# Kernel optimization log

Measured on AMD Instinct MI355X. Metric: run time of the kernel, lower is better.

The kernel has to match this reference:

```python
import jax, jax.numpy as jnp
from jax import lax
import numpy as np

C = 16          # channels
K = 3           # deformable kernel size
PAD = 1


def conv3(x, w, b):
    # 3x3 SAME conv, NCHW / OIHW
    y = lax.conv_general_dilated(x, w, (1, 1), 'SAME',
                                 dimension_numbers=('NCHW', 'OIHW', 'NCHW'))
    return y + b[None, :, None, None]


def deform_conv2d(x, offsets, mask, w, b):
    """torchvision-style modulated deformable conv, stride=1, pad=1, dil=1.
    x: [B,C,H,W]; offsets: [B,2*K*K,H,W] (per-tap y,x interleaved);
    mask: [B,K*K,H,W]; w: [Cout,C,K,K]; b: [Cout]."""
    B, Cin, H, W = x.shape
    ky, kx = jnp.meshgrid(jnp.arange(K), jnp.arange(K), indexing='ij')
    ky = ky.reshape(-1).astype(x.dtype)   # [9]
    kx = kx.reshape(-1).astype(x.dtype)
    off = offsets.reshape(B, K * K, 2, H, W)  # off[:,k,0]=dy, off[:,k,1]=dx
    hh = jnp.arange(H, dtype=x.dtype)
    ww = jnp.arange(W, dtype=x.dtype)
    py = hh[None, None, :, None] + (ky - PAD)[None, :, None, None] + off[:, :, 0]  # [B,9,H,W]
    px = ww[None, None, None, :] + (kx - PAD)[None, :, None, None] + off[:, :, 1]
    y0 = jnp.floor(py)
    x0 = jnp.floor(px)
    dy = py - y0
    dx = px - x0

    def sample_one(img, y0b, x0b, dyb, dxb):
        # img [C,H,W]; y0b/x0b/dyb/dxb [9,H,W]
        y0i = y0b.astype(jnp.int32)
        x0i = x0b.astype(jnp.int32)

        def gather(yi, xi):
            valid = ((yi >= 0) & (yi < H) & (xi >= 0) & (xi < W)).astype(img.dtype)
            yc = jnp.clip(yi, 0, H - 1)
            xc = jnp.clip(xi, 0, W - 1)
            return img[:, yc, xc] * valid[None]   # [C,9,H,W]

        v00 = gather(y0i,     x0i)
        v01 = gather(y0i,     x0i + 1)
        v10 = gather(y0i + 1, x0i)
        v11 = gather(y0i + 1, x0i + 1)
        return (v00 * (1 - dyb) * (1 - dxb) + v01 * (1 - dyb) * dxb
                + v10 * dyb * (1 - dxb) + v11 * dyb * dxb)   # [C,9,H,W]

    sampled = jax.vmap(sample_one)(x, y0, x0, dy, dx)          # [B,C,9,H,W]
    sampled = sampled * mask[:, None]                           # modulate
    out = jnp.einsum('bckhw,ock->bohw', sampled, w.reshape(w.shape[0], Cin, K * K))
    return out + b[None, :, None, None]


def setup_inputs() -> dict:
    key = jax.random.key(0)
    ks = iter(jax.random.split(key, 32))

    def w(shape, scale=0.1):
        return (jax.random.normal(next(ks), shape, dtype=jnp.float32) * scale)

    B, H, W = 4, 256, 256
    d = {
        'f_E': jax.random.normal(next(ks), (B, C, H, W), dtype=jnp.float32),
        'f_F': jax.random.normal(next(ks), (B, C, H, W), dtype=jnp.float32),
        # SpatialAttentionBlock
        'sab_att_w1': w((C, 2 * C, 3, 3)), 'sab_att_b1': w((C,)),
        'sab_att_w2': w((1, C, 3, 3)),      'sab_att_b2': w((1,)),
        'sab_ref_w':  w((C, 2 * C, 3, 3)),  'sab_ref_b':  w((C,)),
        # DeformableConvLayer offset/mask net (last layer small -> modest offsets)
        'om_w1': w((C, 2 * C, 3, 3)),       'om_b1': w((C,)),
        'om_w2': w((C, C, 3, 3)),           'om_b2': w((C,)),
        'om_w3': w((3 * K * K, C, 3, 3), 0.05), 'om_b3': w((3 * K * K,), 0.05),
        # deformable conv weight/bias
        'dcb_w': w((C, C, 3, 3)),           'dcb_b': w((C,)),
        # refinements
        'dcbref_w': w((C, 2 * C, 3, 3)),    'dcbref_b': w((C,)),
        'fin_w':    w((C, 2 * C, 3, 3)),    'fin_b':    w((C,)),
    }
    return d


def reference(f_E, f_F,
              sab_att_w1, sab_att_b1, sab_att_w2, sab_att_b2,
              sab_ref_w, sab_ref_b,
              om_w1, om_b1, om_w2, om_b2, om_w3, om_b3,
              dcb_w, dcb_b, dcbref_w, dcbref_b, fin_w, fin_b):
    relu = jax.nn.relu
    # --- SAB branch: sab(f_E, f_F) ---
    comb = jnp.concatenate([f_E, f_F], axis=1)
    M_E = jax.nn.sigmoid(conv3(relu(conv3(comb, sab_att_w1, sab_att_b1)),
                               sab_att_w2, sab_att_b2))          # [B,1,H,W]
    f_Esa = f_E * M_E
    f_EFsa = relu(conv3(jnp.concatenate([f_Esa, f_F], axis=1), sab_ref_w, sab_ref_b))
    # --- DCB branch: dcb_layer(f_F, f_E) -> deform on f_E, cat([f_E, f_F]) ---
    comb2 = jnp.concatenate([f_E, f_F], axis=1)
    om = conv3(relu(conv3(relu(conv3(comb2, om_w1, om_b1)), om_w2, om_b2)),
               om_w3, om_b3)                                      # [B,27,H,W]
    offsets = om[:, :2 * K * K]
    mask = jax.nn.sigmoid(om[:, 2 * K * K:])
    f_Edc = relu(deform_conv2d(f_E, offsets, mask, dcb_w, dcb_b))
    f_EFdc = relu(conv3(jnp.concatenate([f_Edc, f_F], axis=1), dcbref_w, dcbref_b))
    # --- final fusion ---
    f_EF = relu(conv3(jnp.concatenate([f_EFsa, f_EFdc], axis=1), fin_w, fin_b))
    return f_EF
```

## Files before the change

kernel.cpp:

```cpp
#include <hip/hip_runtime.h>
#include <cstdint>
#include <cstddef>

#define HH 256
#define WW 256
#define HWW (HH * WW)

typedef __attribute__((ext_vector_type(8))) short bf16x8;
typedef __attribute__((ext_vector_type(4))) float f32x4;

__device__ inline unsigned short f2bf(float f) {
  unsigned u = __float_as_uint(f);
  unsigned r = (u + 0x7fffu + ((u >> 16) & 1u)) >> 16;
  return (unsigned short)r;
}
__device__ inline float bf2f(unsigned short u) {
  return __uint_as_float((unsigned)u << 16);
}
__device__ inline float bf_lo(unsigned w) { return __uint_as_float(w << 16); }
__device__ inline float bf_hi(unsigned w) { return __uint_as_float(w & 0xffff0000u); }

struct RD { const float* src; void* dst; int cin, cout, mode; };
struct RA { RD d[9]; };

__device__ void repack_one(const RD& t) {
  if (t.mode == 2) {
    const int NST = (t.cin * 9 + 31) / 32;
    const int OT = (t.cout + 15) / 16;
    const int n = OT * NST * 512;
    unsigned short* dst = (unsigned short*)t.dst;
    for (int i = threadIdx.x; i < n; i += 256) {
      int j = i & 7;
      int l = (i >> 3) & 63;
      int rest = i >> 9;
      int s = rest % NST;
      int ot = rest / NST;
      int o = ot * 16 + (l & 15);
      int klin = s * 32 + ((l >> 4) << 3) + j;
      int tap = klin / t.cin;
      int c = klin % t.cin;
      float v = 0.f;
      if (tap < 9 && o < t.cout) v = t.src[(o * t.cin + c) * 9 + tap];
      dst[i] = f2bf(v);
    }
  } else {
    float* dst = (float*)t.dst;
    const int n = t.cin * t.cout * 9;
    for (int i = threadIdx.x; i < n; i += 256) {
      int k = i % 9;
      int rest = i / 9;
      int c = rest % t.cin;
      int o = rest / t.cin;
      if (t.mode == 0) dst[(c * 9 + k) * t.cout + o] = t.src[(o * t.cin + c) * 9 + k];
      else             dst[(k * t.cin + c) * t.cout + o] = t.src[(o * t.cin + c) * 9 + k];
    }
  }
}

__global__ __launch_bounds__(256) void prep_k(
    RA ra, const float* __restrict__ fe, const float* __restrict__ ff,
    unsigned short* __restrict__ xe, unsigned short* __restrict__ xf) {
  const int b = blockIdx.z;
  if (blockIdx.x == 256) {
    const int d0 = b * 3;
    for (int d = d0; d < d0 + 3 && d < 9; ++d) repack_one(ra.d[d]);
    return;
  }
  const int pixel = blockIdx.x * 256 + threadIdx.x;
#pragma unroll
  for (int t = 0; t < 2; ++t) {
    const float* src = t ? ff : fe;
    unsigned short* dst = t ? xf : xe;
    unsigned w[8];
#pragma unroll
    for (int j = 0; j < 8; ++j) {
      unsigned short lo = f2bf(src[((size_t)b * 16 + 2 * j) * HWW + pixel]);
      unsigned short hi = f2bf(src[((size_t)b * 16 + 2 * j + 1) * HWW + pixel]);
      w[j] = (unsigned)lo | ((unsigned)hi << 16);
    }
    uint4* d4 = (uint4*)(dst + ((size_t)b * HWW + pixel) * 16);
    d4[0] = make_uint4(w[0], w[1], w[2], w[3]);
    d4[1] = make_uint4(w[4], w[5], w[6], w[7]);
  }
}

template <int NSLOT, int OT, int OUT_MODE, int COUTR>
__global__ __launch_bounds__(256) void conv_nhwc(
    const unsigned short* __restrict__ inA, const unsigned short* __restrict__ inB,
    const unsigned short* __restrict__ wtm, const float* __restrict__ bias,
    void* __restrict__ outv) {
  constexpr int CIN = NSLOT * 8;
  constexpr int NST = (CIN * 9 + 31) / 32;
  constexpr int SHIFT = (NSLOT == 4) ? 1 : 2;
  constexpr int STRIDE = NSLOT * 16;
  constexpr int PX = 34, PY = 10;
  __shared__ __align__(16) char smem[PY * PX * STRIDE];

  const int b = blockIdx.z;
  const int tx0 = blockIdx.x * 32;
  const int ty0 = blockIdx.y * 8;
  const int tid = threadIdx.x;
  const int lane = tid & 63;
  const int wv = tid >> 6;

  bf16x8 afr[OT][NST];
#pragma unroll
  for (int ot = 0; ot < OT; ++ot)
#pragma unroll
    for (int s = 0; s < NST; ++s)
      afr[ot][s] = *(const bf16x8*)(wtm + (size_t)(((ot * NST + s) * 64 + lane) * 8));

  const int px_l = lane & 15;
  const int og = lane >> 4;

  f32x4 acc[4][OT];
#pragma unroll
  for (int ot = 0; ot < OT; ++ot) {
    f32x4 bv;
#pragma unroll
    for (int r = 0; r < 4; ++r) {
      int o = ot * 16 + og * 4 + r;
      bv[r] = bias[o < COUTR ? o : COUTR - 1];
    }
#pragma unroll
    for (int t = 0; t < 4; ++t) acc[t][ot] = bv;
  }

  for (int i = tid; i < PY * PX * NSLOT; i += 256) {
    int pp = i / NSLOT;
    int s = i - pp * NSLOT;
    int ly = pp / PX;
    int lx = pp - ly * PX;
    int gy = ty0 + ly - 1;
    int gx = tx0 + lx - 1;
    uint4 v = make_uint4(0, 0, 0, 0);
    if (gy >= 0 && gy < HH && gx >= 0 && gx < WW) {
      const unsigned short* src = (NSLOT == 2 || s < 2) ? inA : inB;
      int sl = (NSLOT == 4 && s >= 2) ? s - 2 : s;
      v = *(const uint4*)(src + ((size_t)b * HWW + (size_t)gy * WW + gx) * 16 + sl * 8);
    }
    int swz = (s ^ (pp >> SHIFT)) & (NSLOT - 1);
    *(uint4*)(smem + (size_t)pp * STRIDE + (swz << 4)) = v;
  }
  __syncthreads();

  int dpix[NST], dslot[NST];
#pragma unroll
  for (int s = 0; s < NST; ++s) {
    int klin = s * 32 + og * 8;
    int tap = klin / CIN;
    if (tap > 8) tap = 8;
    int coff = klin % CIN;
    dpix[s] = (tap / 3) * PX + (tap % 3);
    dslot[s] = coff >> 3;
  }

  const int oy_l = wv * 2;
#pragma unroll
  for (int t = 0; t < 4; ++t) {
    const int base_pix = (oy_l + (t >> 1)) * PX + (t & 1) * 16 + px_l;
#pragma unroll
    for (int s = 0; s < NST; ++s) {
      int pp = base_pix + dpix[s];
      int off = pp * STRIDE + (((dslot[s] ^ (pp >> SHIFT)) & (NSLOT - 1)) << 4);
      bf16x8 bvv = *(const bf16x8*)(smem + off);
#pragma unroll
      for (int ot = 0; ot < OT; ++ot)
        acc[t][ot] = __builtin_amdgcn_mfma_f32_16x16x32_bf16(afr[ot][s], bvv, acc[t][ot], 0, 0, 0);
    }
  }

#pragma unroll
  for (int t = 0; t < 4; ++t) {
    const int gy = ty0 + oy_l + (t >> 1);
    const int gx = tx0 + (t & 1) * 16 + px_l;
#pragma unroll
    for (int ot = 0; ot < OT; ++ot) {
      const int o0 = ot * 16 + og * 4;
      if (OUT_MODE == 2) {
        unsigned lo = (unsigned)f2bf(fmaxf(acc[t][ot][0], 0.f)) |
                      ((unsigned)f2bf(fmaxf(acc[t][ot][1], 0.f)) << 16);
        unsigned hi = (unsigned)f2bf(fmaxf(acc[t][ot][2], 0.f)) |
                      ((unsigned)f2bf(fmaxf(acc[t][ot][3], 0.f)) << 16);
        uint2* dst = (uint2*)((unsigned short*)outv +
                              ((size_t)b * HWW + (size_t)gy * WW + gx) * 16 + o0);
        *dst = make_uint2(lo, hi);
      } else if (OUT_MODE == 0) {
#pragma unroll
        for (int r = 0; r < 4; ++r) {
          int o = o0 + r;
          if (o < COUTR)
            ((float*)outv)[((size_t)b * COUTR + o) * HWW + (size_t)gy * WW + gx] =
                fmaxf(acc[t][ot][r], 0.f);
        }
      } else {
#pragma unroll
        for (int r = 0; r < 4; ++r) {
          int o = o0 + r;
          if (o < COUTR)
            ((unsigned short*)outv)[((size_t)b * COUTR + o) * HWW + (size_t)gy * WW + gx] =
                f2bf(acc[t][ot][r]);
        }
      }
    }
  }
}

__global__ __launch_bounds__(256) void conv_dual_k(
    const unsigned short* __restrict__ inA, const unsigned short* __restrict__ inB,
    const unsigned short* __restrict__ w1, const float* __restrict__ b1,
    const unsigned short* __restrict__ w2, const float* __restrict__ b2,
    unsigned short* __restrict__ out1, unsigned short* __restrict__ out2) {
  constexpr int NSLOT = 4, NST = 9, SHIFT = 1, STRIDE = 64, PX = 34, PY = 10;
  __shared__ __align__(16) char smem[PY * PX * STRIDE];

  const int b = blockIdx.z;
  const int tx0 = blockIdx.x * 32;
  const int ty0 = blockIdx.y * 8;
  const int tid = threadIdx.x;
  const int lane = tid & 63;
  const int wv = tid >> 6;

  bf16x8 afr1[NST], afr2[NST];
#pragma unroll
  for (int s = 0; s < NST; ++s) {
    afr1[s] = *(const bf16x8*)(w1 + (size_t)((s * 64 + lane) * 8));
    afr2[s] = *(const bf16x8*)(w2 + (size_t)((s * 64 + lane) * 8));
  }

  const int px_l = lane & 15;
  const int og = lane >> 4;

  f32x4 acc1[4], acc2[4];
  {
    f32x4 bv1, bv2;
#pragma unroll
    for (int r = 0; r < 4; ++r) {
      bv1[r] = b1[og * 4 + r];
      bv2[r] = b2[og * 4 + r];
    }
#pragma unroll
    for (int t = 0; t < 4; ++t) { acc1[t] = bv1; acc2[t] = bv2; }
  }

  for (int i = tid; i < PY * PX * NSLOT; i += 256) {
    int pp = i / NSLOT;
    int s = i - pp * NSLOT;
    int ly = pp / PX;
    int lx = pp - ly * PX;
    int gy = ty0 + ly - 1;
    int gx = tx0 + lx - 1;
    uint4 v = make_uint4(0, 0, 0, 0);
    if (gy >= 0 && gy < HH && gx >= 0 && gx < WW) {
      const unsigned short* src = (s < 2) ? inA : inB;
      int sl = (s >= 2) ? s - 2 : s;
      v = *(const uint4*)(src + ((size_t)b * HWW + (size_t)gy * WW + gx) * 16 + sl * 8);
    }
    int swz = (s ^ (pp >> SHIFT)) & 3;
    *(uint4*)(smem + (size_t)pp * STRIDE + (swz << 4)) = v;
  }
  __syncthreads();

  int dpix[NST], dslot[NST];
#pragma unroll
  for (int s = 0; s < NST; ++s) {
    int klin = s * 32 + og * 8;
    int tap = klin / 32;
    int coff = klin % 32;
    dpix[s] = (tap / 3) * PX + (tap % 3);
    dslot[s] = coff >> 3;
  }

  const int oy_l = wv * 2;
#pragma unroll
  for (int t = 0; t < 4; ++t) {
    const int base_pix = (oy_l + (t >> 1)) * PX + (t & 1) * 16 + px_l;
#pragma unroll
    for (int s = 0; s < NST; ++s) {
      int pp = base_pix + dpix[s];
      int off = pp * STRIDE + (((dslot[s] ^ (pp >> SHIFT)) & 3) << 4);
      bf16x8 bvv = *(const bf16x8*)(smem + off);
      acc1[t] = __builtin_amdgcn_mfma_f32_16x16x32_bf16(afr1[s], bvv, acc1[t], 0, 0, 0);
      acc2[t] = __builtin_amdgcn_mfma_f32_16x16x32_bf16(afr2[s], bvv, acc2[t], 0, 0, 0);
    }
  }

#pragma unroll
  for (int t = 0; t < 4; ++t) {
    const int gy = ty0 + oy_l + (t >> 1);
    const int gx = tx0 + (t & 1) * 16 + px_l;
    const size_t base = ((size_t)b * HWW + (size_t)gy * WW + gx) * 16 + og * 4;
    {
      unsigned lo = (unsigned)f2bf(fmaxf(acc1[t][0], 0.f)) |
                    ((unsigned)f2bf(fmaxf(acc1[t][1], 0.f)) << 16);
      unsigned hi = (unsigned)f2bf(fmaxf(acc1[t][2], 0.f)) |
                    ((unsigned)f2bf(fmaxf(acc1[t][3], 0.f)) << 16);
      *(uint2*)(out1 + base) = make_uint2(lo, hi);
    }
    {
      unsigned lo = (unsigned)f2bf(fmaxf(acc2[t][0], 0.f)) |
                    ((unsigned)f2bf(fmaxf(acc2[t][1], 0.f)) << 16);
      unsigned hi = (unsigned)f2bf(fmaxf(acc2[t][2], 0.f)) |
                    ((unsigned)f2bf(fmaxf(acc2[t][3], 0.f)) << 16);
      *(uint2*)(out2 + base) = make_uint2(lo, hi);
    }
  }
}

__global__ __launch_bounds__(256) void sagate_k(
    const unsigned short* __restrict__ xa, const unsigned short* __restrict__ xe,
    const unsigned short* __restrict__ xf,
    const float* __restrict__ gw, const float* __restrict__ gb,
    const unsigned short* __restrict__ wtm, const float* __restrict__ bias,
    unsigned short* __restrict__ out) {
  constexpr int NST = 9, SHIFT = 1, STRIDE = 64, PX = 34, PY = 10;
  __shared__ __align__(16) char smem[PY * PX * STRIDE];

  const int b = blockIdx.z;
  const int tx0 = blockIdx.x * 32;
  const int ty0 = blockIdx.y * 8;
  const int tid = threadIdx.x;
  const int lane = tid & 63;
  const int wv = tid >> 6;

  bf16x8 afr[NST];
#pragma unroll
  for (int s = 0; s < NST; ++s)
    afr[s] = *(const bf16x8*)(wtm + (size_t)((s * 64 + lane) * 8));

  const int px_l = lane & 15;
  const int og = lane >> 4;

  f32x4 acc[4];
  {
    f32x4 bv;
#pragma unroll
    for (int r = 0; r < 4; ++r) bv[r] = bias[og * 4 + r];
#pragma unroll
    for (int t = 0; t < 4; ++t) acc[t] = bv;
  }

  for (int i = tid; i < PY * PX * 2; i += 256) {
    int pp = i >> 1;
    int s = 2 + (i & 1);
    int ly = pp / PX;
    int lx = pp - ly * PX;
    int gy = ty0 + ly - 1;
    int gx = tx0 + lx - 1;
    uint4 v = make_uint4(0, 0, 0, 0);
    if (gy >= 0 && gy < HH && gx >= 0 && gx < WW)
      v = *(const uint4*)(xf + ((size_t)b * HWW + (size_t)gy * WW + gx) * 16 + (s - 2) * 8);
    int swz = (s ^ (pp >> SHIFT)) & 3;
    *(uint4*)(smem + (size_t)pp * STRIDE + (swz << 4)) = v;
  }

  const float gbias = gb[0];
  for (int i = tid; i < PY * PX; i += 256) {
    int ly = i / PX;
    int lx = i - ly * PX;
    int gy = ty0 + ly - 1;
    int gx = tx0 + lx - 1;
    uint4 v0 = make_uint4(0, 0, 0, 0), v1 = make_uint4(0, 0, 0, 0);
    if (gy >= 0 && gy < HH && gx >= 0 && gx < WW) {
      float a = gbias;
#pragma unroll
      for (int ky = 0; ky < 3; ++ky) {
        int ay = gy + ky - 1;
        if (ay < 0 || ay >= HH) continue;
#pragma unroll
        for (int kx = 0; kx < 3; ++kx) {
          int ax = gx + kx - 1;
          if (ax < 0 || ax >= WW) continue;
          const int k = ky * 3 + kx;
          const uint4* p = (const uint4*)(xa + ((size_t)b * HWW + (size_t)ay * WW + ax) * 16);
          uint4 t0 = p[0], t1 = p[1];
          unsigned wv8[8] = {t0.x, t0.y, t0.z, t0.w, t1.x, t1.y, t1.z, t1.w};
#pragma unroll
          for (int j = 0; j < 8; ++j) {
            a = fmaf(bf_lo(wv8[j]), gw[(2 * j) * 9 + k], a);
            a = fmaf(bf_hi(wv8[j]), gw[(2 * j + 1) * 9 + k], a);
          }
        }
      }
      float m = 1.0f / (1.0f + expf(-a));
      const uint4* pe = (const uint4*)(xe + ((size_t)b * HWW + (size_t)gy * WW + gx) * 16);
      uint4 e0 = pe[0], e1 = pe[1];
      unsigned ev[8] = {e0.x, e0.y, e0.z, e0.w, e1.x, e1.y, e1.z, e1.w};
      unsigned r[8];
#pragma unroll
      for (int j = 0; j < 8; ++j) {
        unsigned short lo = f2bf(bf_lo(ev[j]) * m);
        unsigned short hi = f2bf(bf_hi(ev[j]) * m);
        r[j] = (unsigned)lo | ((unsigned)hi << 16);
      }
      v0 = make_uint4(r[0], r[1], r[2], r[3]);
      v1 = make_uint4(r[4], r[5], r[6], r[7]);
    }
    int swz0 = (0 ^ (i >> SHIFT)) & 3;
    int swz1 = (1 ^ (i >> SHIFT)) & 3;
    *(uint4*)(smem + (size_t)i * STRIDE + (swz0 << 4)) = v0;
    *(uint4*)(smem + (size_t)i * STRIDE + (swz1 << 4)) = v1;
  }
  __syncthreads();

  int dpix[NST], dslot[NST];
#pragma unroll
  for (int s = 0; s < NST; ++s) {
    int klin = s * 32 + og * 8;
    int tap = klin / 32;
    int coff = klin % 32;
    dpix[s] = (tap / 3) * PX + (tap % 3);
    dslot[s] = coff >> 3;
  }

  const int oy_l = wv * 2;
#pragma unroll
  for (int t = 0; t < 4; ++t) {
    const int base_pix = (oy_l + (t >> 1)) * PX + (t & 1) * 16 + px_l;
#pragma unroll
    for (int s = 0; s < NST; ++s) {
      int pp = base_pix + dpix[s];
      int off = pp * STRIDE + (((dslot[s] ^ (pp >> SHIFT)) & 3) << 4);
      bf16x8 bvv = *(const bf16x8*)(smem + off);
      acc[t] = __builtin_amdgcn_mfma_f32_16x16x32_bf16(afr[s], bvv, acc[t], 0, 0, 0);
    }
  }

#pragma unroll
  for (int t = 0; t < 4; ++t) {
    const int gy = ty0 + oy_l + (t >> 1);
    const int gx = tx0 + (t & 1) * 16 + px_l;
    unsigned lo = (unsigned)f2bf(fmaxf(acc[t][0], 0.f)) |
                  ((unsigned)f2bf(fmaxf(acc[t][1], 0.f)) << 16);
    unsigned hi = (unsigned)f2bf(fmaxf(acc[t][2], 0.f)) |
                  ((unsigned)f2bf(fmaxf(acc[t][3], 0.f)) << 16);
    *(uint2*)(out + ((size_t)b * HWW + (size_t)gy * WW + gx) * 16 + og * 4) = make_uint2(lo, hi);
  }
}

__global__ __launch_bounds__(256) void deform_v4(
    const unsigned short* __restrict__ xn, const unsigned short* __restrict__ om,
    const float* __restrict__ wt, const float* __restrict__ bias,
    unsigned short* __restrict__ out) {
  const int bid = blockIdx.x;
  const int xcd = bid & 7;
  const int b = xcd >> 1;
  const int pb = ((bid >> 3) << 1) | (xcd & 1);
  const int pixel = pb * 256 + (int)threadIdx.x;
  const int y = pixel >> 8;
  const int xq = pixel & 255;
  const unsigned short* xb = xn + (size_t)b * HWW * 16;
  const unsigned short* omb = om + (size_t)b * 27 * HWW;

  float acc[16];
#pragma unroll
  for (int o = 0; o < 16; ++o) acc[o] = bias[o];

#pragma unroll
  for (int k = 0; k < 9; ++k) {
    float offy = bf2f(omb[(size_t)(2 * k) * HWW + pixel]);
    float offx = bf2f(omb[(size_t)(2 * k + 1) * HWW + pixel]);
    float m = 1.0f / (1.0f + expf(-bf2f(omb[(size_t)(18 + k) * HWW + pixel])));
    float py = (float)y + (float)(k / 3 - 1) + offy;
    float px = (float)xq + (float)(k % 3 - 1) + offx;
    float y0f = floorf(py);
    float x0f = floorf(px);
    float dy = py - y0f;
    float dx = px - x0f;
    int y0 = (int)y0f, x0 = (int)x0f;
    int y1 = y0 + 1, x1 = x0 + 1;
    bool vy0 = (y0 >= 0) && (y0 < HH);
    bool vy1 = (y1 >= 0) && (y1 < HH);
    bool vx0 = (x0 >= 0) && (x0 < WW);
    bool vx1 = (x1 >= 0) && (x1 < WW);
    int yc0 = min(max(y0, 0), HH - 1);
    int yc1 = min(max(y1, 0), HH - 1);
    int xc0 = min(max(x0, 0), WW - 1);
    int xc1 = min(max(x1, 0), WW - 1);
    float w00 = (1.f - dy) * (1.f - dx) * m;
    float w01 = (1.f - dy) * dx * m;
    float w10 = dy * (1.f - dx) * m;
    float w11 = dy * dx * m;
    if (!(vy0 && vx0)) w00 = 0.f;
    if (!(vy0 && vx1)) w01 = 0.f;
    if (!(vy1 && vx0)) w10 = 0.f;
    if (!(vy1 && vx1)) w11 = 0.f;

    const uint4* p00 = (const uint4*)(xb + (size_t)(yc0 * WW + xc0) * 16);
    const uint4* p01 = (const uint4*)(xb + (size_t)(yc0 * WW + xc1) * 16);
    const uint4* p10 = (const uint4*)(xb + (size_t)(yc1 * WW + xc0) * 16);
    const uint4* p11 = (const uint4*)(xb + (size_t)(yc1 * WW + xc1) * 16);
    uint4 a0 = p00[0], a1 = p00[1];
    uint4 b0 = p01[0], b1 = p01[1];
    uint4 c0 = p10[0], c1 = p10[1];
    uint4 d0 = p11[0], d1 = p11[1];
    unsigned wA[8] = {a0.x, a0.y, a0.z, a0.w, a1.x, a1.y, a1.z, a1.w};
    unsigned wB[8] = {b0.x, b0.y, b0.z, b0.w, b1.x, b1.y, b1.z, b1.w};
    unsigned wC[8] = {c0.x, c0.y, c0.z, c0.w, c1.x, c1.y, c1.z, c1.w};
    unsigned wD[8] = {d0.x, d0.y, d0.z, d0.w, d1.x, d1.y, d1.z, d1.w};

    float s[16];
#pragma unroll
    for (int j = 0; j < 8; ++j) {
      s[2 * j]     = bf_lo(wA[j]) * w00 + bf_lo(wB[j]) * w01 + bf_lo(wC[j]) * w10 + bf_lo(wD[j]) * w11;
      s[2 * j + 1] = bf_hi(wA[j]) * w00 + bf_hi(wB[j]) * w01 + bf_hi(wC[j]) * w10 + bf_hi(wD[j]) * w11;
    }
    const float* wk = wt + (size_t)k * 256;
#pragma unroll
    for (int c = 0; c < 16; ++c)
#pragma unroll
      for (int o = 0; o < 16; ++o)
        acc[o] = fmaf(s[c], wk[c * 16 + o], acc[o]);
  }
  unsigned r[8];
#pragma unroll
  for (int j = 0; j < 8; ++j) {
    unsigned short lo = f2bf(fmaxf(acc[2 * j], 0.f));
    unsigned short hi = f2bf(fmaxf(acc[2 * j + 1], 0.f));
    r[j] = (unsigned)lo | ((unsigned)hi << 16);
  }
  uint4* d4 = (uint4*)(out + ((size_t)b * HWW + pixel) * 16);
  d4[0] = make_uint4(r[0], r[1], r[2], r[3]);
  d4[1] = make_uint4(r[4], r[5], r[6], r[7]);
}

extern "C" void kernel_launch(void* const* d_in, const int* in_sizes, int n_in,
                              void* d_out, int out_size, void* d_ws, size_t ws_size,
                              hipStream_t stream) {
  (void)in_sizes; (void)n_in; (void)out_size; (void)ws_size;
  const float* f_E = (const float*)d_in[0];
  const float* f_F = (const float*)d_in[1];
  const float* att_w1 = (const float*)d_in[2];
  const float* att_b1 = (const float*)d_in[3];
  const float* att_w2 = (const float*)d_in[4];
  const float* att_b2 = (const float*)d_in[5];
  const float* ref_w = (const float*)d_in[6];
  const float* ref_b = (const float*)d_in[7];
  const float* om_w1 = (const float*)d_in[8];
  const float* om_b1 = (const float*)d_in[9];
  const float* om_w2 = (const float*)d_in[10];
  const float* om_b2 = (const float*)d_in[11];
  const float* om_w3 = (const float*)d_in[12];
  const float* om_b3 = (const float*)d_in[13];
  const float* dcb_w = (const float*)d_in[14];
  const float* dcb_b = (const float*)d_in[15];
  const float* dcbref_w = (const float*)d_in[16];
  const float* dcbref_b = (const float*)d_in[17];
  const float* fin_w = (const float*)d_in[18];
  const float* fin_b = (const float*)d_in[19];
  float* outp = (float*)d_out;

  const size_t TN = (size_t)4 * HWW * 16;
  unsigned short* XE  = (unsigned short*)d_ws;
  unsigned short* XF  = XE + TN;
  unsigned short* XA  = XF + TN;
  unsigned short* XT  = XA + TN;
  unsigned short* X2  = XT + TN;
  unsigned short* XSA = X2 + TN;
  unsigned short* OMB = XSA + TN;
  unsigned short* WM  = OMB + (size_t)4 * 27 * HWW;

  unsigned short* WM_att1 = WM;
  unsigned short* WM_ref  = WM_att1 + 4608;
  unsigned short* WM_om1  = WM_ref + 4608;
  unsigned short* WM_om2  = WM_om1 + 4608;
  unsigned short* WM_om3  = WM_om2 + 2560;
  unsigned short* WM_dref = WM_om3 + 5120;
  unsigned short* WM_fin  = WM_dref + 4608;
  float* WF_att2 = (float*)(WM_fin + 4608);
  float* WF_dcb  = WF_att2 + 144;

  RA ra;
  ra.d[0] = {att_w1, WM_att1, 32, 16, 2};
  ra.d[1] = {ref_w, WM_ref, 32, 16, 2};
  ra.d[2] = {om_w1, WM_om1, 32, 16, 2};
  ra.d[3] = {om_w2, WM_om2, 16, 16, 2};
  ra.d[4] = {om_w3, WM_om3, 16, 27, 2};
  ra.d[5] = {dcbref_w, WM_dref, 32, 16, 2};
  ra.d[6] = {fin_w, WM_fin, 32, 16, 2};
  ra.d[7] = {att_w2, WF_att2, 16, 1, 0};
  ra.d[8] = {dcb_w, WF_dcb, 16, 16, 1};

  dim3 blk(256);
  prep_k<<<dim3(257, 1, 4), blk, 0, stream>>>(ra, f_E, f_F, XE, XF);

  dim3 gm(WW / 32, HH / 8, 4);

  conv_dual_k<<<gm, blk, 0, stream>>>(XE, XF, WM_att1, att_b1, WM_om1, om_b1, XA, XT);
  sagate_k<<<gm, blk, 0, stream>>>(XA, XE, XF, WF_att2, att_b2, WM_ref, ref_b, X2);
  conv_nhwc<2, 1, 2, 16><<<gm, blk, 0, stream>>>(XT, nullptr, WM_om2, om_b2, XA);
  conv_nhwc<2, 2, 1, 27><<<gm, blk, 0, stream>>>(XA, nullptr, WM_om3, om_b3, OMB);
  deform_v4<<<dim3(1024), blk, 0, stream>>>(XE, OMB, WF_dcb, dcb_b, XSA);
  conv_nhwc<4, 1, 2, 16><<<gm, blk, 0, stream>>>(XSA, XF, WM_dref, dcbref_b, XT);
  conv_nhwc<4, 1, 0, 16><<<gm, blk, 0, stream>>>(X2, XT, WM_fin, fin_b, outp);
}
```

Baseline: 115.4 us.

## Fuse consecutive 3x3 conv pairs into halo-recomputing kernels

Replaces the separate om2→om3 convolutions and the dcbref→final convolutions with two fused kernels. Each computes the first conv over a tile enlarged by a one-pixel halo and keeps the intermediate in LDS, then runs the second conv from LDS. This drops two kernel launches and the global write and read of two intermediate bf16 tensors. In exchange it recomputes halo pixels, uses more shared memory per block (which may lower occupancy), and adds an extra barrier phase.

```diff
diff --git a/kernel.cpp b/kernel.cpp
--- a/kernel.cpp
+++ b/kernel.cpp
@@ -84,128 +84,6 @@
   }
 }
 
-template <int NSLOT, int OT, int OUT_MODE, int COUTR>
-__global__ __launch_bounds__(256) void conv_nhwc(
-    const unsigned short* __restrict__ inA, const unsigned short* __restrict__ inB,
-    const unsigned short* __restrict__ wtm, const float* __restrict__ bias,
-    void* __restrict__ outv) {
-  constexpr int CIN = NSLOT * 8;
-  constexpr int NST = (CIN * 9 + 31) / 32;
-  constexpr int SHIFT = (NSLOT == 4) ? 1 : 2;
-  constexpr int STRIDE = NSLOT * 16;
-  constexpr int PX = 34, PY = 10;
-  __shared__ __align__(16) char smem[PY * PX * STRIDE];
-
-  const int b = blockIdx.z;
-  const int tx0 = blockIdx.x * 32;
-  const int ty0 = blockIdx.y * 8;
-  const int tid = threadIdx.x;
-  const int lane = tid & 63;
-  const int wv = tid >> 6;
-
-  bf16x8 afr[OT][NST];
-#pragma unroll
-  for (int ot = 0; ot < OT; ++ot)
-#pragma unroll
-    for (int s = 0; s < NST; ++s)
-      afr[ot][s] = *(const bf16x8*)(wtm + (size_t)(((ot * NST + s) * 64 + lane) * 8));
-
-  const int px_l = lane & 15;
-  const int og = lane >> 4;
-
-  f32x4 acc[4][OT];
-#pragma unroll
-  for (int ot = 0; ot < OT; ++ot) {
-    f32x4 bv;
-#pragma unroll
-    for (int r = 0; r < 4; ++r) {
-      int o = ot * 16 + og * 4 + r;
-      bv[r] = bias[o < COUTR ? o : COUTR - 1];
-    }
-#pragma unroll
-    for (int t = 0; t < 4; ++t) acc[t][ot] = bv;
-  }
-
-  for (int i = tid; i < PY * PX * NSLOT; i += 256) {
-    int pp = i / NSLOT;
-    int s = i - pp * NSLOT;
-    int ly = pp / PX;
-    int lx = pp - ly * PX;
-    int gy = ty0 + ly - 1;
-    int gx = tx0 + lx - 1;
-    uint4 v = make_uint4(0, 0, 0, 0);
-    if (gy >= 0 && gy < HH && gx >= 0 && gx < WW) {
-      const unsigned short* src = (NSLOT == 2 || s < 2) ? inA : inB;
-      int sl = (NSLOT == 4 && s >= 2) ? s - 2 : s;
-      v = *(const uint4*)(src + ((size_t)b * HWW + (size_t)gy * WW + gx) * 16 + sl * 8);
-    }
-    int swz = (s ^ (pp >> SHIFT)) & (NSLOT - 1);
-    *(uint4*)(smem + (size_t)pp * STRIDE + (swz << 4)) = v;
-  }
-  __syncthreads();
-
-  int dpix[NST], dslot[NST];
-#pragma unroll
-  for (int s = 0; s < NST; ++s) {
-    int klin = s * 32 + og * 8;
-    int tap = klin / CIN;
-    if (tap > 8) tap = 8;
-    int coff = klin % CIN;
-    dpix[s] = (tap / 3) * PX + (tap % 3);
-    dslot[s] = coff >> 3;
-  }
-
-  const int oy_l = wv * 2;
-#pragma unroll
-  for (int t = 0; t < 4; ++t) {
-    const int base_pix = (oy_l + (t >> 1)) * PX + (t & 1) * 16 + px_l;
-#pragma unroll
-    for (int s = 0; s < NST; ++s) {
-      int pp = base_pix + dpix[s];
-      int off = pp * STRIDE + (((dslot[s] ^ (pp >> SHIFT)) & (NSLOT - 1)) << 4);
-      bf16x8 bvv = *(const bf16x8*)(smem + off);
-#pragma unroll
-      for (int ot = 0; ot < OT; ++ot)
-        acc[t][ot] = __builtin_amdgcn_mfma_f32_16x16x32_bf16(afr[ot][s], bvv, acc[t][ot], 0, 0, 0);
-    }
-  }
-
-#pragma unroll
-  for (int t = 0; t < 4; ++t) {
-    const int gy = ty0 + oy_l + (t >> 1);
-    const int gx = tx0 + (t & 1) * 16 + px_l;
-#pragma unroll
-    for (int ot = 0; ot < OT; ++ot) {
-      const int o0 = ot * 16 + og * 4;
-      if (OUT_MODE == 2) {
-        unsigned lo = (unsigned)f2bf(fmaxf(acc[t][ot][0], 0.f)) |
-                      ((unsigned)f2bf(fmaxf(acc[t][ot][1], 0.f)) << 16);
-        unsigned hi = (unsigned)f2bf(fmaxf(acc[t][ot][2], 0.f)) |
-                      ((unsigned)f2bf(fmaxf(acc[t][ot][3], 0.f)) << 16);
-        uint2* dst = (uint2*)((unsigned short*)outv +
-                              ((size_t)b * HWW + (size_t)gy * WW + gx) * 16 + o0);
-        *dst = make_uint2(lo, hi);
-      } else if (OUT_MODE == 0) {
-#pragma unroll
-        for (int r = 0; r < 4; ++r) {
-          int o = o0 + r;
-          if (o < COUTR)
-            ((float*)outv)[((size_t)b * COUTR + o) * HWW + (size_t)gy * WW + gx] =
-                fmaxf(acc[t][ot][r], 0.f);
-        }
-      } else {
-#pragma unroll
-        for (int r = 0; r < 4; ++r) {
-          int o = o0 + r;
-          if (o < COUTR)
-            ((unsigned short*)outv)[((size_t)b * COUTR + o) * HWW + (size_t)gy * WW + gx] =
-                f2bf(acc[t][ot][r]);
-        }
-      }
-    }
-  }
-}
-
 __global__ __launch_bounds__(256) void conv_dual_k(
     const unsigned short* __restrict__ inA, const unsigned short* __restrict__ inB,
     const unsigned short* __restrict__ w1, const float* __restrict__ b1,
@@ -435,6 +313,147 @@
     unsigned hi = (unsigned)f2bf(fmaxf(acc[t][2], 0.f)) |
                   ((unsigned)f2bf(fmaxf(acc[t][3], 0.f)) << 16);
     *(uint2*)(out + ((size_t)b * HWW + (size_t)gy * WW + gx) * 16 + og * 4) = make_uint2(lo, hi);
+  }
+}
+
+__global__ __launch_bounds__(256) void om_fused_k(
+    const unsigned short* __restrict__ xt,
+    const unsigned short* __restrict__ w2m, const float* __restrict__ b2,
+    const unsigned short* __restrict__ w3m, const float* __restrict__ b3,
+    unsigned short* __restrict__ omb) {
+  __shared__ __align__(16) char smem[12 * 36 * 32 + 10 * 34 * 32];
+  char* stage = smem;
+  char* t3 = smem + 12 * 36 * 32;
+
+  const int b = blockIdx.z;
+  const int tx0 = blockIdx.x * 32;
+  const int ty0 = blockIdx.y * 8;
+  const int tid = threadIdx.x;
+  const int lane = tid & 63;
+  const int wv = tid >> 6;
+  const int px_l = lane & 15;
+  const int og = lane >> 4;
+
+  for (int i = tid; i < 12 * 36 * 2; i += 256) {
+    int pp = i >> 1;
+    int s = i & 1;
+    int lr = pp / 36;
+    int lc = pp - lr * 36;
+    int gy = ty0 + lr - 2;
+    int gx = tx0 + lc - 2;
+    uint4 v = make_uint4(0, 0, 0, 0);
+    if (gy >= 0 && gy < HH && gx >= 0 && gx < WW)
+      v = *(const uint4*)(xt + ((size_t)b * HWW + (size_t)gy * WW + gx) * 16 + s * 8);
+    int swz = (s ^ (pp >> 2)) & 1;
+    *(uint4*)(stage + (size_t)pp * 32 + (swz << 4)) = v;
+  }
+  __syncthreads();
+
+  {
+    bf16x8 afr1[5];
+#pragma unroll
+    for (int s = 0; s < 5; ++s)
+      afr1[s] = *(const bf16x8*)(w2m + (size_t)((s * 64 + lane) * 8));
+    f32x4 bvec;
+#pragma unroll
+    for (int r = 0; r < 4; ++r) bvec[r] = b2[og * 4 + r];
+    int tap1[5], slot1[5];
+#pragma unroll
+    for (int s = 0; s < 5; ++s) {
+      int klin = s * 32 + og * 8;
+      int tap = klin / 16;
+      if (tap > 8) tap = 8;
+      int coff = klin % 16;
+      tap1[s] = (tap / 3) * 36 + (tap % 3);
+      slot1[s] = coff >> 3;
+    }
+    for (int f = wv; f < 22; f += 4) {
+      int p = f * 16 + px_l;
+      int r = p / 34;
+      int c = p - r * 34;
+      f32x4 acc = bvec;
+#pragma unroll
+      for (int s = 0; s < 5; ++s) {
+        int pp2 = r * 36 + c + tap1[s];
+        int off = pp2 * 32 + (((slot1[s] ^ (pp2 >> 2)) & 1) << 4);
+        bf16x8 bv = *(const bf16x8*)(stage + off);
+        acc = __builtin_amdgcn_mfma_f32_16x16x32_bf16(afr1[s], bv, acc, 0, 0, 0);
+      }
+      if (p < 340) {
+        int gy = ty0 + r - 1;
+        int gx = tx0 + c - 1;
+        unsigned lo = 0, hi = 0;
+        if (gy >= 0 && gy < HH && gx >= 0 && gx < WW) {
+          lo = (unsigned)f2bf(fmaxf(acc[0], 0.f)) | ((unsigned)f2bf(fmaxf(acc[1], 0.f)) << 16);
+          hi = (unsigned)f2bf(fmaxf(acc[2], 0.f)) | ((unsigned)f2bf(fmaxf(acc[3], 0.f)) << 16);
+        }
+        int slot = og >> 1;
+        int off = p * 32 + (((slot ^ (p >> 2)) & 1) << 4) + (og & 1) * 8;
+        *(uint2*)(t3 + off) = make_uint2(lo, hi);
+      }
+    }
+  }
+  __syncthreads();
+
+  bf16x8 afr2[2][5];
+#pragma unroll
+  for (int ot = 0; ot < 2; ++ot)
+#pragma unroll
+    for (int s = 0; s < 5; ++s)
+      afr2[ot][s] = *(const bf16x8*)(w3m + (size_t)(((ot * 5 + s) * 64 + lane) * 8));
+
+  f32x4 acc2[4][2];
+#pragma unroll
+  for (int ot = 0; ot < 2; ++ot) {
+    f32x4 bv;
+#pragma unroll
+    for (int r = 0; r < 4; ++r) {
+      int o = ot * 16 + og * 4 + r;
+      bv[r] = b3[o < 27 ? o : 26];
+    }
+#pragma unroll
+    for (int t = 0; t < 4; ++t) acc2[t][ot] = bv;
+  }
+
+  int tap2[5], slot2[5];
+#pragma unroll
+  for (int s = 0; s < 5; ++s) {
+    int klin = s * 32 + og * 8;
+    int tap = klin / 16;
+    if (tap > 8) tap = 8;
+    int coff = klin % 16;
+    tap2[s] = (tap / 3) * 34 + (tap % 3);
+    slot2[s] = coff >> 3;
+  }
+
+  const int oy_l = wv * 2;
+#pragma unroll
+  for (int t = 0; t < 4; ++t) {
+    const int base_pix = (oy_l + (t >> 1)) * 34 + (t & 1) * 16 + px_l;
+#pragma unroll
+    for (int s = 0; s < 5; ++s) {
+      int pp = base_pix + tap2[s];
+      int off = pp * 32 + (((slot2[s] ^ (pp >> 2)) & 1) << 4);
+      bf16x8 bv = *(const bf16x8*)(t3 + off);
+      acc2[t][0] = __builtin_amdgcn_mfma_f32_16x16x32_bf16(afr2[0][s], bv, acc2[t][0], 0, 0, 0);
+      acc2[t][1] = __builtin_amdgcn_mfma_f32_16x16x32_bf16(afr2[1][s], bv, acc2[t][1], 0, 0, 0);
+    }
+  }
+
+#pragma unroll
+  for (int t = 0; t < 4; ++t) {
+    const int gy = ty0 + oy_l + (t >> 1);
+    const int gx = tx0 + (t & 1) * 16 + px_l;
+#pragma unroll
+    for (int ot = 0; ot < 2; ++ot) {
+      const int o0 = ot * 16 + og * 4;
+#pragma unroll
+      for (int r = 0; r < 4; ++r) {
+        int o = o0 + r;
+        if (o < 27)
+          omb[((size_t)b * 27 + o) * HWW + (size_t)gy * WW + gx] = f2bf(acc2[t][ot][r]);
+      }
+    }
   }
 }
 
@@ -524,6 +543,154 @@
   d4[1] = make_uint4(r[4], r[5], r[6], r[7]);
 }
 
+__global__ __launch_bounds__(256) void fin_fused_k(
+    const unsigned short* __restrict__ xsa, const unsigned short* __restrict__ xf,
+    const unsigned short* __restrict__ wdm, const float* __restrict__ bd,
+    const unsigned short* __restrict__ x2,
+    const unsigned short* __restrict__ wfm, const float* __restrict__ bfv,
+    float* __restrict__ outp) {
+  __shared__ __align__(16) char smem[12 * 36 * 64 + 10 * 34 * 32];
+  char* stage = smem;
+  char* dtile = smem + 12 * 36 * 64;
+  char* x2tile = smem;
+
+  const int b = blockIdx.z;
+  const int tx0 = blockIdx.x * 32;
+  const int ty0 = blockIdx.y * 8;
+  const int tid = threadIdx.x;
+  const int lane = tid & 63;
+  const int wv = tid >> 6;
+  const int px_l = lane & 15;
+  const int og = lane >> 4;
+
+  for (int i = tid; i < 12 * 36 * 4; i += 256) {
+    int pp = i >> 2;
+    int s = i & 3;
+    int lr = pp / 36;
+    int lc = pp - lr * 36;
+    int gy = ty0 + lr - 2;
+    int gx = tx0 + lc - 2;
+    uint4 v = make_uint4(0, 0, 0, 0);
+    if (gy >= 0 && gy < HH && gx >= 0 && gx < WW) {
+      const unsigned short* src = (s < 2) ? xsa : xf;
+      int sl = (s >= 2) ? s - 2 : s;
+      v = *(const uint4*)(src + ((size_t)b * HWW + (size_t)gy * WW + gx) * 16 + sl * 8);
+    }
+    int swz = (s ^ (pp >> 1)) & 3;
+    *(uint4*)(stage + (size_t)pp * 64 + (swz << 4)) = v;
+  }
+  __syncthreads();
+
+  {
+    bf16x8 afr1[9];
+#pragma unroll
+    for (int s = 0; s < 9; ++s)
+      afr1[s] = *(const bf16x8*)(wdm + (size_t)((s * 64 + lane) * 8));
+    f32x4 bvec;
+#pragma unroll
+    for (int r = 0; r < 4; ++r) bvec[r] = bd[og * 4 + r];
+    int tap1[9], slot1[9];
+#pragma unroll
+    for (int s = 0; s < 9; ++s) {
+      int klin = s * 32 + og * 8;
+      int tap = klin / 32;
+      int coff = klin % 32;
+      tap1[s] = (tap / 3) * 36 + (tap % 3);
+      slot1[s] = coff >> 3;
+    }
+    for (int f = wv; f < 22; f += 4) {
+      int p = f * 16 + px_l;
+      int r = p / 34;
+      int c = p - r * 34;
+      f32x4 acc = bvec;
+#pragma unroll
+      for (int s = 0; s < 9; ++s) {
+        int pp2 = r * 36 + c + tap1[s];
+        int off = pp2 * 64 + (((slot1[s] ^ (pp2 >> 1)) & 3) << 4);
+        bf16x8 bv = *(const bf16x8*)(stage + off);
+        acc = __builtin_amdgcn_mfma_f32_16x16x32_bf16(afr1[s], bv, acc, 0, 0, 0);
+      }
+      if (p < 340) {
+        int gy = ty0 + r - 1;
+        int gx = tx0 + c - 1;
+        unsigned lo = 0, hi = 0;
+        if (gy >= 0 && gy < HH && gx >= 0 && gx < WW) {
+          lo = (unsigned)f2bf(fmaxf(acc[0], 0.f)) | ((unsigned)f2bf(fmaxf(acc[1], 0.f)) << 16);
+          hi = (unsigned)f2bf(fmaxf(acc[2], 0.f)) | ((unsigned)f2bf(fmaxf(acc[3], 0.f)) << 16);
+        }
+        int slot = og >> 1;
+        int off = p * 32 + (((slot ^ (p >> 2)) & 1) << 4) + (og & 1) * 8;
+        *(uint2*)(dtile + off) = make_uint2(lo, hi);
+      }
+    }
+  }
+  __syncthreads();
+
+  for (int i = tid; i < 340 * 2; i += 256) {
+    int pp = i >> 1;
+    int s = i & 1;
+    int r = pp / 34;
+    int c = pp - r * 34;
+    int gy = ty0 + r - 1;
+    int gx = tx0 + c - 1;
+    uint4 v = make_uint4(0, 0, 0, 0);
+    if (gy >= 0 && gy < HH && gx >= 0 && gx < WW)
+      v = *(const uint4*)(x2 + ((size_t)b * HWW + (size_t)gy * WW + gx) * 16 + s * 8);
+    int swz = (s ^ (pp >> 2)) & 1;
+    *(uint4*)(x2tile + (size_t)pp * 32 + (swz << 4)) = v;
+  }
+  __syncthreads();
+
+  bf16x8 afr2[9];
+#pragma unroll
+  for (int s = 0; s < 9; ++s)
+    afr2[s] = *(const bf16x8*)(wfm + (size_t)((s * 64 + lane) * 8));
+
+  f32x4 acc2[4];
+  {
+    f32x4 bv;
+#pragma unroll
+    for (int r = 0; r < 4; ++r) bv[r] = bfv[og * 4 + r];
+#pragma unroll
+    for (int t = 0; t < 4; ++t) acc2[t] = bv;
+  }
+
+  int tap2[9], slot2[9];
+#pragma unroll
+  for (int s = 0; s < 9; ++s) {
+    int klin = s * 32 + og * 8;
+    int tap = klin / 32;
+    int coff = klin % 32;
+    tap2[s] = (tap / 3) * 34 + (tap % 3);
+    slot2[s] = coff >> 3;
+  }
+
+  const int oy_l = wv * 2;
+#pragma unroll
+  for (int t = 0; t < 4; ++t) {
+    const int base_pix = (oy_l + (t >> 1)) * 34 + (t & 1) * 16 + px_l;
+#pragma unroll
+    for (int s = 0; s < 9; ++s) {
+      int pp = base_pix + tap2[s];
+      const char* basep = (slot2[s] < 2) ? x2tile : dtile;
+      int sl = slot2[s] & 1;
+      int off = pp * 32 + (((sl ^ (pp >> 2)) & 1) << 4);
+      bf16x8 bv = *(const bf16x8*)(basep + off);
+      acc2[t] = __builtin_amdgcn_mfma_f32_16x16x32_bf16(afr2[s], bv, acc2[t], 0, 0, 0);
+    }
+  }
+
+#pragma unroll
+  for (int t = 0; t < 4; ++t) {
+    const int gy = ty0 + oy_l + (t >> 1);
+    const int gx = tx0 + (t & 1) * 16 + px_l;
+    const int o0 = og * 4;
+#pragma unroll
+    for (int r = 0; r < 4; ++r)
+      outp[((size_t)b * 16 + o0 + r) * HWW + (size_t)gy * WW + gx] = fmaxf(acc2[t][r], 0.f);
+  }
+}
+
 extern "C" void kernel_launch(void* const* d_in, const int* in_sizes, int n_in,
                               void* d_out, int out_size, void* d_ws, size_t ws_size,
                               hipStream_t stream) {
@@ -588,9 +755,7 @@
 
   conv_dual_k<<<gm, blk, 0, stream>>>(XE, XF, WM_att1, att_b1, WM_om1, om_b1, XA, XT);
   sagate_k<<<gm, blk, 0, stream>>>(XA, XE, XF, WF_att2, att_b2, WM_ref, ref_b, X2);
-  conv_nhwc<2, 1, 2, 16><<<gm, blk, 0, stream>>>(XT, nullptr, WM_om2, om_b2, XA);
-  conv_nhwc<2, 2, 1, 27><<<gm, blk, 0, stream>>>(XA, nullptr, WM_om3, om_b3, OMB);
+  om_fused_k<<<gm, blk, 0, stream>>>(XT, WM_om2, om_b2, WM_om3, om_b3, OMB);
   deform_v4<<<dim3(1024), blk, 0, stream>>>(XE, OMB, WF_dcb, dcb_b, XSA);
-  conv_nhwc<4, 1, 2, 16><<<gm, blk, 0, stream>>>(XSA, XF, WM_dref, dcbref_b, XT);
-  conv_nhwc<4, 1, 0, 16><<<gm, blk, 0, stream>>>(X2, XT, WM_fin, fin_b, outp);
-}
+  fin_fused_k<<<gm, blk, 0, stream>>>(XSA, XF, WM_dref, dcbref_b, X2, WM_fin, fin_b, outp);
+}
```

Measured after the change: 109.2 us. -5.4%, faster.
